# Performance work log

Hardware: AMD Instinct MI355X
Metric: run time of the kernel (lower is better)

Reference implementation:

```python
import jax, jax.numpy as jnp
import numpy as np

B, T, F, H, A, DFF, DEMO, NH = 64, 96, 48, 128, 8, 512, 12, 4
DM = H  # d_model == hidden_dim


def _linear(x, W, b):
    # torch nn.Linear: y = x @ W.T + b, W: [out, in]
    return jnp.einsum('...i,oi->...o', x, W) + b


def _layernorm(x, a, b, eps=1e-7):
    # matches the custom LayerNorm: unbiased std (torch.std default)
    mean = x.mean(-1, keepdims=True)
    std = jnp.std(x, axis=-1, keepdims=True, ddof=1)
    return a * (x - mean) / (std + eps) + b


def _forward(x, demo, gru_Wih, gru_Whh, gru_bih, gru_bhh, att_Wt, att_Wx, att_rate,
             demoW, demob, mWq, mbq, mWk, mbk, mWv, mbv, mWo, mbo,
             ln1_a, ln1_b, ln2_a, ln2_b, ffn_W1, ffn_b1, ffn_W2, ffn_b2,
             fWq, fbq, fWk, fbk, fWv, fbv, outW, outb):
    Bs, Ts, Fs = x.shape
    Hd = gru_Whh.shape[-1]

    # ---- per-feature GRUs (input size 1), vectorized over the F features ----
    def step(h, xt):  # h: [B,F,H], xt: [B,F]
        gi = xt[:, :, None] * gru_Wih[None] + gru_bih[None]            # [B,F,3H]
        gh = jnp.einsum('bfh,fgh->bfg', h, gru_Whh) + gru_bhh[None]    # [B,F,3H]
        ir, iz, inn = jnp.split(gi, 3, -1)
        hr, hz, hn = jnp.split(gh, 3, -1)
        r = jax.nn.sigmoid(ir + hr)
        z = jax.nn.sigmoid(iz + hz)
        n = jnp.tanh(inn + r * hn)
        hnew = (1.0 - z) * n + z * h
        return hnew, hnew

    h0 = jnp.zeros((Bs, Fs, Hd), x.dtype)
    _, Hs = jax.lax.scan(step, h0, jnp.moveaxis(x, 1, 0))  # [T,B,F,H]
    Hs = jnp.moveaxis(Hs, 0, 1)                            # [B,T,F,H]

    # ---- time-aware per-feature attention (SingleAttentionPerFeatureNew) ----
    q = jnp.einsum('bfh,fha->bfa', Hs[:, -1], att_Wt)      # query from last step
    k = jnp.einsum('btfh,fha->btfa', Hs, att_Wx)
    dot = jnp.einsum('bfa,btfa->btf', q, k)                # [B,T,F]
    b_time = jnp.arange(Ts, 0, -1, dtype=x.dtype)[None, :, None]  # T..1
    sr = jax.nn.sigmoid(att_rate)[None, None, :]
    sd = jax.nn.sigmoid(dot)
    denom = sr * (jnp.log(2.72 + (1.0 - sd)) * b_time)
    e = jax.nn.relu(sd / denom)
    a = jax.nn.softmax(e, axis=1)                          # softmax over time
    v = jnp.einsum('btf,btfh->bfh', a, Hs)                 # [B,F,H]

    # ---- demographics channel + concat ----
    demo_main = jnp.tanh(_linear(demo, demoW, demob))[:, None, :]
    posi = jnp.concatenate([v, demo_main], axis=1)         # [B,F+1,H]

    # ---- MHA sublayer (pre-norm residual) with DeCov ----
    xn = _layernorm(posi, ln1_a, ln1_b)
    N = xn.shape[1]
    dk = DM // NH
    qh = _linear(xn, mWq, mbq).reshape(Bs, N, NH, dk).transpose(0, 2, 1, 3)
    kh = _linear(xn, mWk, mbk).reshape(Bs, N, NH, dk).transpose(0, 2, 1, 3)
    vh = _linear(xn, mWv, mbv).reshape(Bs, N, NH, dk).transpose(0, 2, 1, 3)
    scores = jnp.einsum('bhnd,bhmd->bhnm', qh, kh) / jnp.sqrt(jnp.asarray(dk, x.dtype))
    p = jax.nn.softmax(scores, axis=-1)
    ctx = jnp.einsum('bhnm,bhmd->bhnd', p, vh).transpose(0, 2, 1, 3).reshape(Bs, N, DM)
    mha_out = _linear(ctx, mWo, mbo)                       # [B,N,DM]

    # DeCov loss: per position n, covariance across batch, off-diagonal Frobenius
    xc = mha_out - mha_out.mean(axis=0, keepdims=True)     # center over batch
    cov = jnp.einsum('bnh,bng->nhg', xc, xc) / (Bs - 1.0)  # [N,H,H]
    diag = jnp.diagonal(cov, axis1=1, axis2=2)             # [N,H]
    decov = 0.5 * (jnp.sum(cov * cov) - jnp.sum(diag * diag))

    h1 = posi + mha_out

    # ---- FFN sublayer (pre-norm residual) ----
    xn2 = _layernorm(h1, ln2_a, ln2_b)
    ffn = _linear(jax.nn.relu(_linear(xn2, ffn_W1, ffn_b1)), ffn_W2, ffn_b2)
    h2 = h1 + ffn

    # ---- FinalAttentionQKV, attention_type='mul' ----
    fq = _linear(h2[:, -1, :], fWq, fbq)                   # [B,DM]
    fk = _linear(h2, fWk, fbk)                             # [B,N,DM]
    fv = _linear(h2, fWv, fbv)
    fe = jnp.einsum('bna,ba->bn', fk, fq)
    alpha = jax.nn.softmax(fe, axis=1)
    pooled = jnp.einsum('bn,bna->ba', alpha, fv)

    out = jax.nn.sigmoid(_linear(pooled, outW, outb))      # [B,1]
    return out, decov


def setup_inputs() -> dict:
    key = jax.random.key(0)
    ks = jax.random.split(key, 40)
    f32 = jnp.float32

    def rn(k, shape, s=0.05):
        return jax.random.normal(k, shape, dtype=f32) * s

    return {
        'x': jax.random.normal(ks[0], (B, T, F), dtype=f32),
        'demo': jax.random.normal(ks[1], (B, DEMO), dtype=f32),
        'gru_Wih': rn(ks[2], (F, 3 * H)),
        'gru_Whh': rn(ks[3], (F, 3 * H, H)),
        'gru_bih': rn(ks[4], (F, 3 * H)),
        'gru_bhh': rn(ks[5], (F, 3 * H)),
        'att_Wt': rn(ks[6], (F, H, A)),
        'att_Wx': rn(ks[7], (F, H, A)),
        'att_rate': jnp.full((F,), 0.8, dtype=f32),
        'demoW': rn(ks[8], (H, DEMO)), 'demob': rn(ks[9], (H,)),
        'mWq': rn(ks[10], (DM, DM)), 'mbq': rn(ks[11], (DM,)),
        'mWk': rn(ks[12], (DM, DM)), 'mbk': rn(ks[13], (DM,)),
        'mWv': rn(ks[14], (DM, DM)), 'mbv': rn(ks[15], (DM,)),
        'mWo': rn(ks[16], (DM, DM)), 'mbo': rn(ks[17], (DM,)),
        'ln1_a': jnp.ones((DM,), dtype=f32), 'ln1_b': jnp.zeros((DM,), dtype=f32),
        'ln2_a': jnp.ones((DM,), dtype=f32), 'ln2_b': jnp.zeros((DM,), dtype=f32),
        'ffn_W1': rn(ks[18], (DFF, DM)), 'ffn_b1': rn(ks[19], (DFF,)),
        'ffn_W2': rn(ks[20], (DM, DFF)), 'ffn_b2': rn(ks[21], (DM,)),
        'fWq': rn(ks[22], (DM, DM)), 'fbq': rn(ks[23], (DM,)),
        'fWk': rn(ks[24], (DM, DM)), 'fbk': rn(ks[25], (DM,)),
        'fWv': rn(ks[26], (DM, DM)), 'fbv': rn(ks[27], (DM,)),
        'outW': rn(ks[28], (1, DM)), 'outb': rn(ks[29], (1,)),
    }


def reference(x, demo, gru_Wih, gru_Whh, gru_bih, gru_bhh, att_Wt, att_Wx, att_rate,
              demoW, demob, mWq, mbq, mWk, mbk, mWv, mbv, mWo, mbo,
              ln1_a, ln1_b, ln2_a, ln2_b, ffn_W1, ffn_b1, ffn_W2, ffn_b2,
              fWq, fbq, fWk, fbk, fWv, fbv, outW, outb):
    return _forward(x, demo, gru_Wih, gru_Whh, gru_bih, gru_bhh, att_Wt, att_Wx, att_rate,
                    demoW, demob, mWq, mbq, mWk, mbk, mWv, mbv, mWo, mbo,
                    ln1_a, ln1_b, ln2_a, ln2_b, ffn_W1, ffn_b1, ffn_W2, ffn_b2,
                    fWq, fbq, fWk, fbk, fWv, fbv, outW, outb)
```

## Files before the change

### kernel.cpp

```cpp
#include <hip/hip_runtime.h>
#include <hip/hip_bf16.h>

namespace {

constexpr int Bc = 64, Tc = 96, Fc = 48, Hc = 128, Ac = 8;
constexpr int DFFc = 512, DEMOc = 12, NHc = 4, Nc = 49, H3c = 384, DKc = 32;

typedef __attribute__((ext_vector_type(8))) short s8v;
typedef __attribute__((ext_vector_type(4))) float f4v;

__device__ __forceinline__ float sigf(float x) { return 1.f / (1.f + expf(-x)); }
__device__ __forceinline__ float sigf_fast(float x) { return 1.f / (1.f + __expf(-x)); }
__device__ __forceinline__ float tanhf_fast(float x) {
  float e = __expf(2.f * x);
  return 1.f - 2.f / (e + 1.f);
}

__device__ __forceinline__ unsigned short f2b(float v) {
  __hip_bfloat16 h = __float2bfloat16(v);
  union { __hip_bfloat16 b; unsigned short u; } c;
  c.b = h;
  return c.u;
}
__device__ __forceinline__ float b2f(unsigned short u) {
  union { unsigned u32; float f; } c;
  c.u32 = (unsigned)u << 16;
  return c.f;
}

template <typename ST> __device__ __forceinline__ void stv(ST* p, float v);
template <> __device__ __forceinline__ void stv<float>(float* p, float v) { *p = v; }
template <> __device__ __forceinline__ void stv<__hip_bfloat16>(__hip_bfloat16* p, float v) {
  *p = __float2bfloat16(v);
}

template <typename ST> __device__ __forceinline__ void ld4(const ST* p, float* o);
template <> __device__ __forceinline__ void ld4<float>(const float* p, float* o) {
  float4 v = *reinterpret_cast<const float4*>(p);
  o[0] = v.x; o[1] = v.y; o[2] = v.z; o[3] = v.w;
}
template <> __device__ __forceinline__ void ld4<__hip_bfloat16>(const __hip_bfloat16* p, float* o) {
  ushort4 v = *reinterpret_cast<const ushort4*>(p);
  union { unsigned u; float f; } t;
  t.u = (unsigned)v.x << 16; o[0] = t.f;
  t.u = (unsigned)v.y << 16; o[1] = t.f;
  t.u = (unsigned)v.z << 16; o[2] = t.f;
  t.u = (unsigned)v.w << 16; o[3] = t.f;
}

__device__ __forceinline__ float bsum(float v, float* red, int nw) {
#pragma unroll
  for (int off = 32; off > 0; off >>= 1) v += __shfl_down(v, off);
  int lane = threadIdx.x & 63, wid = threadIdx.x >> 6;
  __syncthreads();
  if (lane == 0) red[wid] = v;
  __syncthreads();
  float s = 0.f;
  for (int i = 0; i < nw; i++) s += red[i];
  return s;
}

template <typename ST>
__global__ __launch_bounds__(512, 2) void gru_mfma(
    const float* __restrict__ x, const float* __restrict__ Wih,
    const float* __restrict__ Whh, const float* __restrict__ bih,
    const float* __restrict__ bhh, ST* __restrict__ Hs, float* __restrict__ hT) {
  const int f = blockIdx.x;
  const int b0 = blockIdx.y << 4;
  const int tid = threadIdx.x;
  const int lane = tid & 63;
  const int w = tid >> 6;
  const int hh = (w << 4) + (lane & 15);
  const int lg = lane >> 4;

  s8v wh[12], wl[12];
#pragma unroll
  for (int gate = 0; gate < 3; gate++) {
#pragma unroll
    for (int ks = 0; ks < 4; ks++) {
      const float* wp = Whh + ((size_t)f * H3c + gate * Hc + hh) * Hc + (ks << 5) + (lg << 3);
      s8v hi, lo;
#pragma unroll
      for (int j = 0; j < 8; j++) {
        float v = wp[j];
        unsigned short hb = f2b(v);
        unsigned short lb = f2b(v - b2f(hb));
        hi[j] = (short)hb;
        lo[j] = (short)lb;
      }
      wh[gate * 4 + ks] = hi;
      wl[gate * 4 + ks] = lo;
    }
  }

  const float wi0 = Wih[f * H3c + hh], wi1 = Wih[f * H3c + Hc + hh], wi2 = Wih[f * H3c + 2 * Hc + hh];
  const float bi0 = bih[f * H3c + hh], bi1 = bih[f * H3c + Hc + hh], bi2 = bih[f * H3c + 2 * Hc + hh];
  const float bh0 = bhh[f * H3c + hh], bh1 = bhh[f * H3c + Hc + hh], bh2 = bhh[f * H3c + 2 * Hc + hh];

  __shared__ unsigned short hbuf[2][2][16 * 128];
  __shared__ float xs[16][100];

  {
    unsigned short* hz = &hbuf[0][0][0];
    for (int i = tid; i < 2 * 2 * 16 * 128; i += 512) hz[i] = 0;
    for (int i = tid; i < 16 * Tc; i += 512) {
      int b = i / Tc, t = i - b * Tc;
      xs[b][t] = x[((size_t)(b0 + b) * Tc + t) * Fc + f];
    }
  }
  __syncthreads();

  float hold[4] = {0.f, 0.f, 0.f, 0.f};
  int cur = 0;

  for (int t = 0; t < Tc; t++) {
    s8v ahi[4], alo[4];
#pragma unroll
    for (int ks = 0; ks < 4; ks++) {
      int m = lane & 15;
      int idx = m * 128 + ((((ks << 2) + lg) ^ (m & 7)) << 3);
      ahi[ks] = *reinterpret_cast<const s8v*>(&hbuf[cur][0][idx]);
      alo[ks] = *reinterpret_cast<const s8v*>(&hbuf[cur][1][idx]);
    }
    f4v accr = {0.f, 0.f, 0.f, 0.f}, accz = {0.f, 0.f, 0.f, 0.f}, accn = {0.f, 0.f, 0.f, 0.f};
#pragma unroll
    for (int ks = 0; ks < 4; ks++) {
      accr = __builtin_amdgcn_mfma_f32_16x16x32_bf16(ahi[ks], wh[0 + ks], accr, 0, 0, 0);
      accz = __builtin_amdgcn_mfma_f32_16x16x32_bf16(ahi[ks], wh[4 + ks], accz, 0, 0, 0);
      accn = __builtin_amdgcn_mfma_f32_16x16x32_bf16(ahi[ks], wh[8 + ks], accn, 0, 0, 0);
      accr = __builtin_amdgcn_mfma_f32_16x16x32_bf16(alo[ks], wh[0 + ks], accr, 0, 0, 0);
      accz = __builtin_amdgcn_mfma_f32_16x16x32_bf16(alo[ks], wh[4 + ks], accz, 0, 0, 0);
      accn = __builtin_amdgcn_mfma_f32_16x16x32_bf16(alo[ks], wh[8 + ks], accn, 0, 0, 0);
      accr = __builtin_amdgcn_mfma_f32_16x16x32_bf16(ahi[ks], wl[0 + ks], accr, 0, 0, 0);
      accz = __builtin_amdgcn_mfma_f32_16x16x32_bf16(ahi[ks], wl[4 + ks], accz, 0, 0, 0);
      accn = __builtin_amdgcn_mfma_f32_16x16x32_bf16(ahi[ks], wl[8 + ks], accn, 0, 0, 0);
    }
    int nxt = cur ^ 1;
#pragma unroll
    for (int r = 0; r < 4; r++) {
      int bt = (lg << 2) + r;
      float xv = xs[bt][t];
      float rr = sigf_fast(xv * wi0 + bi0 + accr[r] + bh0);
      float zz = sigf_fast(xv * wi1 + bi1 + accz[r] + bh1);
      float nn = tanhf_fast(xv * wi2 + bi2 + rr * (accn[r] + bh2));
      float hn = (1.f - zz) * nn + zz * hold[r];
      hold[r] = hn;
      stv(&Hs[(((size_t)(b0 + bt) * Tc + t) * Fc + f) * Hc + hh], hn);
      unsigned short hb = f2b(hn);
      unsigned short lb = f2b(hn - b2f(hb));
      int widx = bt * 128 + (((hh >> 3) ^ (bt & 7)) << 3) + (hh & 7);
      hbuf[nxt][0][widx] = hb;
      hbuf[nxt][1][widx] = lb;
    }
    cur = nxt;
    __syncthreads();
  }
#pragma unroll
  for (int r = 0; r < 4; r++) {
    int bt = (lg << 2) + r;
    hT[((size_t)(b0 + bt) * Fc + f) * Hc + hh] = hold[r];
  }
}

template <typename ST>
__global__ __launch_bounds__(256) void feat_attn(
    const ST* __restrict__ Hs, const float* __restrict__ hT,
    const float* __restrict__ Wt, const float* __restrict__ Wx,
    const float* __restrict__ rate, float* __restrict__ posi) {
  const int f = blockIdx.x, b = blockIdx.y;
  const int tid = threadIdx.x;
  __shared__ float tile[Tc][Hc + 1];
  __shared__ float wxs[Hc][Ac];
  __shared__ float qs[Ac];
  __shared__ float es[Tc];
  __shared__ float red[2];

  for (int i = tid; i < Tc * (Hc / 4); i += 256) {
    int t = i >> 5, k = (i & 31) << 2;
    float o[4];
    ld4(&Hs[(((size_t)b * Tc + t) * Fc + f) * Hc + k], o);
    tile[t][k] = o[0]; tile[t][k + 1] = o[1]; tile[t][k + 2] = o[2]; tile[t][k + 3] = o[3];
  }
  for (int i = tid; i < Hc * Ac; i += 256) (&wxs[0][0])[i] = Wx[(size_t)f * Hc * Ac + i];
  if (tid < Ac) {
    float q = 0.f;
    const float* hTp = hT + ((size_t)b * Fc + f) * Hc;
    for (int h = 0; h < Hc; h++) q += hTp[h] * Wt[((size_t)f * Hc + h) * Ac + tid];
    qs[tid] = q;
  }
  __syncthreads();
  if (tid < Tc) {
    float ka[Ac];
#pragma unroll
    for (int a = 0; a < Ac; a++) ka[a] = 0.f;
    for (int h = 0; h < Hc; h++) {
      float hv = tile[tid][h];
#pragma unroll
      for (int a = 0; a < Ac; a++) ka[a] += hv * wxs[h][a];
    }
    float dot = 0.f;
#pragma unroll
    for (int a = 0; a < Ac; a++) dot += qs[a] * ka[a];
    float sd = sigf(dot);
    float denom = sigf(rate[f]) * (logf(2.72f + (1.f - sd)) * (float)(Tc - tid));
    es[tid] = fmaxf(sd / denom, 0.f);
  }
  __syncthreads();
  if (tid == 0) {
    float m = -1e30f;
    for (int t = 0; t < Tc; t++) m = fmaxf(m, es[t]);
    red[0] = m;
  }
  __syncthreads();
  if (tid < Tc) es[tid] = expf(es[tid] - red[0]);
  __syncthreads();
  if (tid == 0) {
    float s = 0.f;
    for (int t = 0; t < Tc; t++) s += es[t];
    red[1] = 1.f / s;
  }
  __syncthreads();
  if (tid < Hc) {
    float acc = 0.f;
    for (int t = 0; t < Tc; t++) acc += es[t] * tile[t][tid];
    posi[((size_t)b * Nc + f) * Hc + tid] = acc * red[1];
  }
}

__global__ __launch_bounds__(128) void demo_k(
    const float* __restrict__ demo, const float* __restrict__ dW,
    const float* __restrict__ db, float* __restrict__ posi) {
  int b = blockIdx.x, h = threadIdx.x;
  float acc = db[h];
  const float* dp = demo + b * DEMOc;
  const float* wp = dW + h * DEMOc;
#pragma unroll
  for (int d = 0; d < DEMOc; d++) acc += dp[d] * wp[d];
  posi[((size_t)b * Nc + (Nc - 1)) * Hc + h] = tanhf(acc);
}

__global__ __launch_bounds__(128) void ln_qkv(
    const float* __restrict__ posi, const float* __restrict__ ga, const float* __restrict__ be,
    const float* __restrict__ Wq, const float* __restrict__ bq,
    const float* __restrict__ Wk, const float* __restrict__ bk,
    const float* __restrict__ Wv, const float* __restrict__ bv,
    float* __restrict__ qb, float* __restrict__ kb, float* __restrict__ vb) {
  int bn = blockIdx.x;
  int b = bn / Nc, n = bn % Nc;
  int h = threadIdx.x;
  __shared__ float xn[Hc];
  __shared__ float red[2];
  float xv = posi[(size_t)bn * Hc + h];
  float m = bsum(xv, red, 2) * (1.f / Hc);
  float d = xv - m;
  float var = bsum(d * d, red, 2) * (1.f / (Hc - 1));
  xn[h] = ga[h] * d / (sqrtf(var) + 1e-7f) + be[h];
  __syncthreads();
  float q = bq[h], k = bk[h], v = bv[h];
  for (int kk = 0; kk < Hc; kk++) {
    float xk = xn[kk];
    q += xk * Wq[h * Hc + kk];
    k += xk * Wk[h * Hc + kk];
    v += xk * Wv[h * Hc + kk];
  }
  int head = h >> 5, dd = h & 31;
  size_t o = (((size_t)b * NHc + head) * Nc + n) * DKc + dd;
  qb[o] = q; kb[o] = k; vb[o] = v;
}

__global__ __launch_bounds__(64) void mha_attn(
    const float* __restrict__ qb, const float* __restrict__ kb,
    const float* __restrict__ vb, float* __restrict__ ctx) {
  int hd = blockIdx.x, b = blockIdx.y;
  int tid = threadIdx.x;
  __shared__ float ksm[Nc][DKc];
  __shared__ float vsm[Nc][DKc];
  __shared__ float sc[Nc][Nc];
  size_t base = ((size_t)b * NHc + hd) * Nc * DKc;
  for (int i = tid; i < Nc * DKc; i += 64) {
    ksm[i / DKc][i % DKc] = kb[base + i];
    vsm[i / DKc][i % DKc] = vb[base + i];
  }
  __syncthreads();
  if (tid < Nc) {
    float qr[DKc];
#pragma unroll
    for (int d = 0; d < DKc; d++) qr[d] = qb[base + tid * DKc + d];
    float mx = -1e30f;
    for (int mm = 0; mm < Nc; mm++) {
      float s = 0.f;
#pragma unroll
      for (int d = 0; d < DKc; d++) s += qr[d] * ksm[mm][d];
      s *= 0.17677669529663687f;
      sc[tid][mm] = s;
      mx = fmaxf(mx, s);
    }
    float ssum = 0.f;
    for (int mm = 0; mm < Nc; mm++) {
      float e = expf(sc[tid][mm] - mx);
      sc[tid][mm] = e;
      ssum += e;
    }
    float inv = 1.f / ssum;
    float acc[DKc];
#pragma unroll
    for (int d = 0; d < DKc; d++) acc[d] = 0.f;
    for (int mm = 0; mm < Nc; mm++) {
      float p = sc[tid][mm] * inv;
#pragma unroll
      for (int d = 0; d < DKc; d++) acc[d] += p * vsm[mm][d];
    }
    float* cp = ctx + ((size_t)b * Nc + tid) * Hc + hd * DKc;
#pragma unroll
    for (int d = 0; d < DKc; d++) cp[d] = acc[d];
  }
}

__global__ __launch_bounds__(128) void wo_res(
    const float* __restrict__ ctx, const float* __restrict__ Wo,
    const float* __restrict__ bo, const float* __restrict__ posi,
    float* __restrict__ mha, float* __restrict__ h1) {
  int bn = blockIdx.x;
  int h = threadIdx.x;
  __shared__ float cs[Hc];
  cs[h] = ctx[(size_t)bn * Hc + h];
  __syncthreads();
  float acc = bo[h];
  for (int k = 0; k < Hc; k++) acc += cs[k] * Wo[h * Hc + k];
  mha[(size_t)bn * Hc + h] = acc;
  h1[(size_t)bn * Hc + h] = posi[(size_t)bn * Hc + h] + acc;
}

__global__ __launch_bounds__(512) void decov_k(
    const float* __restrict__ mha, float* __restrict__ dacc) {
  int n = blockIdx.x;
  int tid = threadIdx.x;
  __shared__ float xc[Bc][Hc];
  __shared__ float red[8];
  for (int i = tid; i < Bc * Hc; i += 512) {
    int b = i >> 7, h = i & 127;
    xc[b][h] = mha[((size_t)b * Nc + n) * Hc + h];
  }
  __syncthreads();
  if (tid < Hc) {
    float s = 0.f;
    for (int b = 0; b < Bc; b++) s += xc[b][tid];
    s *= (1.f / Bc);
    for (int b = 0; b < Bc; b++) xc[b][tid] -= s;
  }
  __syncthreads();
  float p2 = 0.f, pd = 0.f;
  for (int e = tid; e < Hc * Hc; e += 512) {
    int hh = e >> 7, gg = e & 127;
    float c = 0.f;
    for (int b = 0; b < Bc; b++) c += xc[b][hh] * xc[b][gg];
    c *= (1.f / (Bc - 1));
    float c2 = c * c;
    p2 += c2;
    if (hh == gg) pd += c2;
  }
  float s2 = bsum(p2, red, 8);
  float sdg = bsum(pd, red, 8);
  if (tid == 0) atomicAdd(dacc, 0.5f * (s2 - sdg));
}

__global__ __launch_bounds__(256) void ln2_ffn1(
    const float* __restrict__ h1, const float* __restrict__ ga, const float* __restrict__ be,
    const float* __restrict__ W1, const float* __restrict__ b1, float* __restrict__ t1) {
  int bn = blockIdx.x;
  int tid = threadIdx.x;
  __shared__ float xn[Hc];
  __shared__ float red[4];
  float xv = (tid < Hc) ? h1[(size_t)bn * Hc + tid] : 0.f;
  float m = bsum(xv, red, 4) * (1.f / Hc);
  float d = (tid < Hc) ? (xv - m) : 0.f;
  float var = bsum(d * d, red, 4) * (1.f / (Hc - 1));
  if (tid < Hc) xn[tid] = ga[tid] * d / (sqrtf(var) + 1e-7f) + be[tid];
  __syncthreads();
#pragma unroll
  for (int jj = 0; jj < 2; jj++) {
    int j = tid + jj * 256;
    float acc = b1[j];
    for (int k = 0; k < Hc; k++) acc += xn[k] * W1[j * Hc + k];
    t1[(size_t)bn * DFFc + j] = fmaxf(acc, 0.f);
  }
}

__global__ __launch_bounds__(128) void ffn2_res(
    const float* __restrict__ t1, const float* __restrict__ W2,
    const float* __restrict__ b2, const float* __restrict__ h1, float* __restrict__ h2) {
  int bn = blockIdx.x;
  int h = threadIdx.x;
  __shared__ float ts[DFFc];
  for (int i = h; i < DFFc; i += 128) ts[i] = t1[(size_t)bn * DFFc + i];
  __syncthreads();
  float acc = b2[h];
  for (int j = 0; j < DFFc; j++) acc += ts[j] * W2[h * DFFc + j];
  h2[(size_t)bn * Hc + h] = h1[(size_t)bn * Hc + h] + acc;
}

__global__ __launch_bounds__(128) void final_fkv(
    const float* __restrict__ h2,
    const float* __restrict__ Wk, const float* __restrict__ bk,
    const float* __restrict__ Wv, const float* __restrict__ bv,
    const float* __restrict__ Wq, const float* __restrict__ bq,
    float* __restrict__ fkb, float* __restrict__ fvb, float* __restrict__ fqb) {
  int bn = blockIdx.x;
  int b = bn / Nc, n = bn - b * Nc;
  int h = threadIdx.x;
  __shared__ float xs[Hc];
  xs[h] = h2[(size_t)bn * Hc + h];
  __syncthreads();
  float k = bk[h], v = bv[h];
  const float* wkp = Wk + h * Hc;
  const float* wvp = Wv + h * Hc;
  for (int kk = 0; kk < Hc; kk++) {
    float xv = xs[kk];
    k += xv * wkp[kk];
    v += xv * wvp[kk];
  }
  fkb[(size_t)bn * Hc + h] = k;
  fvb[(size_t)bn * Hc + h] = v;
  if (n == Nc - 1) {
    float q = bq[h];
    const float* wqp = Wq + h * Hc;
    for (int kk = 0; kk < Hc; kk++) q += xs[kk] * wqp[kk];
    fqb[(size_t)b * Hc + h] = q;
  }
}

__global__ __launch_bounds__(128) void final2(
    const float* __restrict__ fkb, const float* __restrict__ fvb,
    const float* __restrict__ fqb,
    const float* __restrict__ oW, const float* __restrict__ ob,
    const float* __restrict__ dacc, float* __restrict__ out) {
  int b = blockIdx.x, h = threadIdx.x;
  int lane = h & 63, wid = h >> 6;
  __shared__ float fqs[Hc];
  __shared__ float alphas[Nc];
  __shared__ float red[2];
  __shared__ float r2[2];
  fqs[h] = fqb[(size_t)b * Hc + h];
  __syncthreads();
  for (int n = wid; n < Nc; n += 2) {
    const float* fkp = fkb + ((size_t)b * Nc + n) * Hc;
    float s = fkp[lane] * fqs[lane] + fkp[lane + 64] * fqs[lane + 64];
#pragma unroll
    for (int off = 32; off > 0; off >>= 1) s += __shfl_down(s, off);
    if (lane == 0) alphas[n] = s;
  }
  __syncthreads();
  if (h == 0) {
    float m = -1e30f;
    for (int n = 0; n < Nc; n++) m = fmaxf(m, alphas[n]);
    float ssum = 0.f;
    for (int n = 0; n < Nc; n++) {
      float e = expf(alphas[n] - m);
      alphas[n] = e;
      ssum += e;
    }
    red[0] = 1.f / ssum;
  }
  __syncthreads();
  float inv = red[0];
  float pv = 0.f;
  for (int n = 0; n < Nc; n++) pv += alphas[n] * fvb[((size_t)b * Nc + n) * Hc + h];
  pv *= inv;
  float c = pv * oW[h];
#pragma unroll
  for (int off = 32; off > 0; off >>= 1) c += __shfl_down(c, off);
  if (lane == 0) r2[wid] = c;
  __syncthreads();
  if (h == 0) {
    out[b] = sigf(r2[0] + r2[1] + ob[0]);
    if (b == 0) out[Bc] = dacc[0];
  }
}

}

extern "C" void kernel_launch(void* const* d_in, const int* in_sizes, int n_in,
                              void* d_out, int out_size, void* d_ws, size_t ws_size,
                              hipStream_t stream) {
  const float* x    = (const float*)d_in[0];
  const float* demo = (const float*)d_in[1];
  const float* gWih = (const float*)d_in[2];
  const float* gWhh = (const float*)d_in[3];
  const float* gbih = (const float*)d_in[4];
  const float* gbhh = (const float*)d_in[5];
  const float* aWt  = (const float*)d_in[6];
  const float* aWx  = (const float*)d_in[7];
  const float* aRt  = (const float*)d_in[8];
  const float* dW   = (const float*)d_in[9];
  const float* db   = (const float*)d_in[10];
  const float* mWq  = (const float*)d_in[11];
  const float* mbq  = (const float*)d_in[12];
  const float* mWk  = (const float*)d_in[13];
  const float* mbk  = (const float*)d_in[14];
  const float* mWv  = (const float*)d_in[15];
  const float* mbv  = (const float*)d_in[16];
  const float* mWo  = (const float*)d_in[17];
  const float* mbo  = (const float*)d_in[18];
  const float* l1a  = (const float*)d_in[19];
  const float* l1b  = (const float*)d_in[20];
  const float* l2a  = (const float*)d_in[21];
  const float* l2b  = (const float*)d_in[22];
  const float* fW1  = (const float*)d_in[23];
  const float* fb1  = (const float*)d_in[24];
  const float* fW2  = (const float*)d_in[25];
  const float* fb2  = (const float*)d_in[26];
  const float* fWq  = (const float*)d_in[27];
  const float* fbq  = (const float*)d_in[28];
  const float* fWk  = (const float*)d_in[29];
  const float* fbk  = (const float*)d_in[30];
  const float* fWv  = (const float*)d_in[31];
  const float* fbv  = (const float*)d_in[32];
  const float* oW   = (const float*)d_in[33];
  const float* ob   = (const float*)d_in[34];

  char* base = (char*)d_ws;
  size_t off = 0;
  auto take = [&](size_t nfloats) -> float* {
    float* r = (float*)(base + off);
    off += ((nfloats * sizeof(float)) + 255) & ~(size_t)255;
    return r;
  };
  float* dec  = take(64);
  float* hT   = take((size_t)Bc * Fc * Hc);
  float* posi = take((size_t)Bc * Nc * Hc);
  float* qb   = take((size_t)Bc * Nc * Hc);
  float* kb   = take((size_t)Bc * Nc * Hc);
  float* vb   = take((size_t)Bc * Nc * Hc);
  float* ctx  = take((size_t)Bc * Nc * Hc);
  float* mha  = take((size_t)Bc * Nc * Hc);
  float* h1   = take((size_t)Bc * Nc * Hc);
  float* t1   = take((size_t)Bc * Nc * DFFc);
  float* h2   = take((size_t)Bc * Nc * Hc);
  float* fkb  = take((size_t)Bc * Nc * Hc);
  float* fvb  = take((size_t)Bc * Nc * Hc);
  float* fqb  = take((size_t)Bc * Hc);
  size_t HsElems = (size_t)Bc * Tc * Fc * Hc;
  void* HsPtr = (void*)(base + off);
  bool f32path = (ws_size >= off + HsElems * sizeof(float));

  hipMemsetAsync(dec, 0, sizeof(float), stream);

  dim3 gGru(Fc, Bc / 16);
  dim3 gAtt(Fc, Bc);
  if (f32path) {
    gru_mfma<float><<<gGru, 512, 0, stream>>>(x, gWih, gWhh, gbih, gbhh, (float*)HsPtr, hT);
    feat_attn<float><<<gAtt, 256, 0, stream>>>((const float*)HsPtr, hT, aWt, aWx, aRt, posi);
  } else {
    gru_mfma<__hip_bfloat16><<<gGru, 512, 0, stream>>>(x, gWih, gWhh, gbih, gbhh,
                                                       (__hip_bfloat16*)HsPtr, hT);
    feat_attn<__hip_bfloat16><<<gAtt, 256, 0, stream>>>((const __hip_bfloat16*)HsPtr, hT,
                                                        aWt, aWx, aRt, posi);
  }
  demo_k<<<Bc, 128, 0, stream>>>(demo, dW, db, posi);
  ln_qkv<<<Bc * Nc, 128, 0, stream>>>(posi, l1a, l1b, mWq, mbq, mWk, mbk, mWv, mbv, qb, kb, vb);
  mha_attn<<<dim3(NHc, Bc), 64, 0, stream>>>(qb, kb, vb, ctx);
  wo_res<<<Bc * Nc, 128, 0, stream>>>(ctx, mWo, mbo, posi, mha, h1);
  decov_k<<<Nc, 512, 0, stream>>>(mha, dec);
  ln2_ffn1<<<Bc * Nc, 256, 0, stream>>>(h1, l2a, l2b, fW1, fb1, t1);
  ffn2_res<<<Bc * Nc, 128, 0, stream>>>(t1, fW2, fb2, h1, h2);
  final_fkv<<<Bc * Nc, 128, 0, stream>>>(h2, fWk, fbk, fWv, fbv, fWq, fbq, fkb, fvb, fqb);
  final2<<<Bc, 128, 0, stream>>>(fkb, fvb, fqb, oW, ob, dec, (float*)d_out);
}
```

Measured before the change: 773.2 us.

## Vectorize dense dot products, parallelize attention reductions, split decov, lighter GRU barrier

```diff
diff --git a/kernel.cpp b/kernel.cpp
--- a/kernel.cpp
+++ b/kernel.cpp
@@ -26,6 +26,36 @@
   union { unsigned u32; float f; } c;
   c.u32 = (unsigned)u << 16;
   return c.f;
+}
+
+__device__ __forceinline__ void lds_barrier() {
+  asm volatile("s_waitcnt lgkmcnt(0)" ::: "memory");
+  __builtin_amdgcn_sched_barrier(0);
+  __builtin_amdgcn_s_barrier();
+  __builtin_amdgcn_sched_barrier(0);
+}
+
+__device__ __forceinline__ float dot128(const float* __restrict__ a,
+                                        const float* __restrict__ w) {
+  float s0 = 0.f, s1 = 0.f, s2 = 0.f, s3 = 0.f;
+#pragma unroll
+  for (int k = 0; k < 128; k += 4) {
+    float4 av = *reinterpret_cast<const float4*>(a + k);
+    float4 wv = *reinterpret_cast<const float4*>(w + k);
+    s0 += av.x * wv.x; s1 += av.y * wv.y; s2 += av.z * wv.z; s3 += av.w * wv.w;
+  }
+  return (s0 + s1) + (s2 + s3);
+}
+__device__ __forceinline__ float dot512(const float* __restrict__ a,
+                                        const float* __restrict__ w) {
+  float s0 = 0.f, s1 = 0.f, s2 = 0.f, s3 = 0.f;
+#pragma unroll 8
+  for (int k = 0; k < 512; k += 4) {
+    float4 av = *reinterpret_cast<const float4*>(a + k);
+    float4 wv = *reinterpret_cast<const float4*>(w + k);
+    s0 += av.x * wv.x; s1 += av.y * wv.y; s2 += av.z * wv.z; s3 += av.w * wv.w;
+  }
+  return (s0 + s1) + (s2 + s3);
 }
 
 template <typename ST> __device__ __forceinline__ void stv(ST* p, float v);
@@ -153,7 +183,7 @@
       hbuf[nxt][1][widx] = lb;
     }
     cur = nxt;
-    __syncthreads();
+    lds_barrier();
   }
 #pragma unroll
   for (int r = 0; r < 4; r++) {
@@ -169,11 +199,14 @@
     const float* __restrict__ rate, float* __restrict__ posi) {
   const int f = blockIdx.x, b = blockIdx.y;
   const int tid = threadIdx.x;
+  const int lane = tid & 63, wid = tid >> 6;
   __shared__ float tile[Tc][Hc + 1];
   __shared__ float wxs[Hc][Ac];
   __shared__ float qs[Ac];
   __shared__ float es[Tc];
-  __shared__ float red[2];
+  __shared__ float qpart[2][Ac];
+  __shared__ float red[4];
+  __shared__ float inv_s;
 
   for (int i = tid; i < Tc * (Hc / 4); i += 256) {
     int t = i >> 5, k = (i & 31) << 2;
@@ -182,12 +215,18 @@
     tile[t][k] = o[0]; tile[t][k + 1] = o[1]; tile[t][k + 2] = o[2]; tile[t][k + 3] = o[3];
   }
   for (int i = tid; i < Hc * Ac; i += 256) (&wxs[0][0])[i] = Wx[(size_t)f * Hc * Ac + i];
-  if (tid < Ac) {
-    float q = 0.f;
-    const float* hTp = hT + ((size_t)b * Fc + f) * Hc;
-    for (int h = 0; h < Hc; h++) q += hTp[h] * Wt[((size_t)f * Hc + h) * Ac + tid];
-    qs[tid] = q;
-  }
+  if (tid < Hc) {
+    float hv = hT[((size_t)b * Fc + f) * Hc + tid];
+#pragma unroll
+    for (int a = 0; a < Ac; a++) {
+      float p = hv * Wt[((size_t)f * Hc + tid) * Ac + a];
+#pragma unroll
+      for (int off = 32; off > 0; off >>= 1) p += __shfl_down(p, off);
+      if (lane == 0) qpart[wid][a] = p;
+    }
+  }
+  __syncthreads();
+  if (tid < Ac) qs[tid] = qpart[0][tid] + qpart[1][tid];
   __syncthreads();
   if (tid < Tc) {
     float ka[Ac];
@@ -206,24 +245,31 @@
     es[tid] = fmaxf(sd / denom, 0.f);
   }
   __syncthreads();
-  if (tid == 0) {
-    float m = -1e30f;
-    for (int t = 0; t < Tc; t++) m = fmaxf(m, es[t]);
-    red[0] = m;
-  }
-  __syncthreads();
-  if (tid < Tc) es[tid] = expf(es[tid] - red[0]);
-  __syncthreads();
-  if (tid == 0) {
-    float s = 0.f;
-    for (int t = 0; t < Tc; t++) s += es[t];
-    red[1] = 1.f / s;
-  }
+  float mv = (tid < Tc) ? es[tid] : -1e30f;
+#pragma unroll
+  for (int off = 32; off > 0; off >>= 1) mv = fmaxf(mv, __shfl_down(mv, off));
+  if (lane == 0) red[wid] = mv;
+  __syncthreads();
+  float m = fmaxf(fmaxf(red[0], red[1]), fmaxf(red[2], red[3]));
+  float ev = (tid < Tc) ? __expf(es[tid] - m) : 0.f;
+  if (tid < Tc) es[tid] = ev;
+#pragma unroll
+  for (int off = 32; off > 0; off >>= 1) ev += __shfl_down(ev, off);
+  __syncthreads();
+  if (lane == 0) red[wid] = ev;
+  __syncthreads();
+  if (tid == 0) inv_s = 1.f / (red[0] + red[1] + red[2] + red[3]);
   __syncthreads();
   if (tid < Hc) {
-    float acc = 0.f;
-    for (int t = 0; t < Tc; t++) acc += es[t] * tile[t][tid];
-    posi[((size_t)b * Nc + f) * Hc + tid] = acc * red[1];
+    float s0 = 0.f, s1 = 0.f, s2 = 0.f, s3 = 0.f;
+#pragma unroll
+    for (int t = 0; t < Tc; t += 4) {
+      s0 += es[t] * tile[t][tid];
+      s1 += es[t + 1] * tile[t + 1][tid];
+      s2 += es[t + 2] * tile[t + 2][tid];
+      s3 += es[t + 3] * tile[t + 3][tid];
+    }
+    posi[((size_t)b * Nc + f) * Hc + tid] = ((s0 + s1) + (s2 + s3)) * inv_s;
   }
 }
 
@@ -248,7 +294,7 @@
   int bn = blockIdx.x;
   int b = bn / Nc, n = bn % Nc;
   int h = threadIdx.x;
-  __shared__ float xn[Hc];
+  __shared__ __align__(16) float xn[Hc];
   __shared__ float red[2];
   float xv = posi[(size_t)bn * Hc + h];
   float m = bsum(xv, red, 2) * (1.f / Hc);
@@ -256,13 +302,9 @@
   float var = bsum(d * d, red, 2) * (1.f / (Hc - 1));
   xn[h] = ga[h] * d / (sqrtf(var) + 1e-7f) + be[h];
   __syncthreads();
-  float q = bq[h], k = bk[h], v = bv[h];
-  for (int kk = 0; kk < Hc; kk++) {
-    float xk = xn[kk];
-    q += xk * Wq[h * Hc + kk];
-    k += xk * Wk[h * Hc + kk];
-    v += xk * Wv[h * Hc + kk];
-  }
+  float q = bq[h] + dot128(xn, Wq + h * Hc);
+  float k = bk[h] + dot128(xn, Wk + h * Hc);
+  float v = bv[h] + dot128(xn, Wv + h * Hc);
   int head = h >> 5, dd = h & 31;
   size_t o = (((size_t)b * NHc + head) * Nc + n) * DKc + dd;
   qb[o] = q; kb[o] = k; vb[o] = v;
@@ -322,18 +364,17 @@
     float* __restrict__ mha, float* __restrict__ h1) {
   int bn = blockIdx.x;
   int h = threadIdx.x;
-  __shared__ float cs[Hc];
+  __shared__ __align__(16) float cs[Hc];
   cs[h] = ctx[(size_t)bn * Hc + h];
   __syncthreads();
-  float acc = bo[h];
-  for (int k = 0; k < Hc; k++) acc += cs[k] * Wo[h * Hc + k];
+  float acc = bo[h] + dot128(cs, Wo + h * Hc);
   mha[(size_t)bn * Hc + h] = acc;
   h1[(size_t)bn * Hc + h] = posi[(size_t)bn * Hc + h] + acc;
 }
 
 __global__ __launch_bounds__(512) void decov_k(
     const float* __restrict__ mha, float* __restrict__ dacc) {
-  int n = blockIdx.x;
+  int n = blockIdx.x, q = blockIdx.y;
   int tid = threadIdx.x;
   __shared__ float xc[Bc][Hc];
   __shared__ float red[8];
@@ -350,14 +391,20 @@
   }
   __syncthreads();
   float p2 = 0.f, pd = 0.f;
-  for (int e = tid; e < Hc * Hc; e += 512) {
-    int hh = e >> 7, gg = e & 127;
-    float c = 0.f;
-    for (int b = 0; b < Bc; b++) c += xc[b][hh] * xc[b][gg];
-    c *= (1.f / (Bc - 1));
-    float c2 = c * c;
-    p2 += c2;
-    if (hh == gg) pd += c2;
+  for (int e = tid; e < 32 * Hc; e += 512) {
+    int hh = (q << 5) + (e >> 7), gg = e & 127;
+    float c0 = 0.f, c1 = 0.f, c2 = 0.f, c3 = 0.f;
+#pragma unroll 4
+    for (int b = 0; b < Bc; b += 4) {
+      c0 += xc[b][hh] * xc[b][gg];
+      c1 += xc[b + 1][hh] * xc[b + 1][gg];
+      c2 += xc[b + 2][hh] * xc[b + 2][gg];
+      c3 += xc[b + 3][hh] * xc[b + 3][gg];
+    }
+    float c = ((c0 + c1) + (c2 + c3)) * (1.f / (Bc - 1));
+    float cc = c * c;
+    p2 += cc;
+    if (hh == gg) pd += cc;
   }
   float s2 = bsum(p2, red, 8);
   float sdg = bsum(pd, red, 8);
@@ -369,7 +416,7 @@
     const float* __restrict__ W1, const float* __restrict__ b1, float* __restrict__ t1) {
   int bn = blockIdx.x;
   int tid = threadIdx.x;
-  __shared__ float xn[Hc];
+  __shared__ __align__(16) float xn[Hc];
   __shared__ float red[4];
   float xv = (tid < Hc) ? h1[(size_t)bn * Hc + tid] : 0.f;
   float m = bsum(xv, red, 4) * (1.f / Hc);
@@ -380,8 +427,7 @@
 #pragma unroll
   for (int jj = 0; jj < 2; jj++) {
     int j = tid + jj * 256;
-    float acc = b1[j];
-    for (int k = 0; k < Hc; k++) acc += xn[k] * W1[j * Hc + k];
+    float acc = b1[j] + dot128(xn, W1 + j * Hc);
     t1[(size_t)bn * DFFc + j] = fmaxf(acc, 0.f);
   }
 }
@@ -391,11 +437,10 @@
     const float* __restrict__ b2, const float* __restrict__ h1, float* __restrict__ h2) {
   int bn = blockIdx.x;
   int h = threadIdx.x;
-  __shared__ float ts[DFFc];
+  __shared__ __align__(16) float ts[DFFc];
   for (int i = h; i < DFFc; i += 128) ts[i] = t1[(size_t)bn * DFFc + i];
   __syncthreads();
-  float acc = b2[h];
-  for (int j = 0; j < DFFc; j++) acc += ts[j] * W2[h * DFFc + j];
+  float acc = b2[h] + dot512(ts, W2 + h * DFFc);
   h2[(size_t)bn * Hc + h] = h1[(size_t)bn * Hc + h] + acc;
 }
 
@@ -408,24 +453,13 @@
   int bn = blockIdx.x;
   int b = bn / Nc, n = bn - b * Nc;
   int h = threadIdx.x;
-  __shared__ float xs[Hc];
+  __shared__ __align__(16) float xs[Hc];
   xs[h] = h2[(size_t)bn * Hc + h];
   __syncthreads();
-  float k = bk[h], v = bv[h];
-  const float* wkp = Wk + h * Hc;
-  const float* wvp = Wv + h * Hc;
-  for (int kk = 0; kk < Hc; kk++) {
-    float xv = xs[kk];
-    k += xv * wkp[kk];
-    v += xv * wvp[kk];
-  }
-  fkb[(size_t)bn * Hc + h] = k;
-  fvb[(size_t)bn * Hc + h] = v;
+  fkb[(size_t)bn * Hc + h] = bk[h] + dot128(xs, Wk + h * Hc);
+  fvb[(size_t)bn * Hc + h] = bv[h] + dot128(xs, Wv + h * Hc);
   if (n == Nc - 1) {
-    float q = bq[h];
-    const float* wqp = Wq + h * Hc;
-    for (int kk = 0; kk < Hc; kk++) q += xs[kk] * wqp[kk];
-    fqb[(size_t)b * Hc + h] = q;
+    fqb[(size_t)b * Hc + h] = bq[h] + dot128(xs, Wq + h * Hc);
   }
 }
 
@@ -560,7 +594,7 @@
   ln_qkv<<<Bc * Nc, 128, 0, stream>>>(posi, l1a, l1b, mWq, mbq, mWk, mbk, mWv, mbv, qb, kb, vb);
   mha_attn<<<dim3(NHc, Bc), 64, 0, stream>>>(qb, kb, vb, ctx);
   wo_res<<<Bc * Nc, 128, 0, stream>>>(ctx, mWo, mbo, posi, mha, h1);
-  decov_k<<<Nc, 512, 0, stream>>>(mha, dec);
+  decov_k<<<dim3(Nc, 4), 512, 0, stream>>>(mha, dec);
   ln2_ffn1<<<Bc * Nc, 256, 0, stream>>>(h1, l2a, l2b, fW1, fb1, t1);
   ffn2_res<<<Bc * Nc, 128, 0, stream>>>(t1, fW2, fb2, h1, h2);
   final_fkv<<<Bc * Nc, 128, 0, stream>>>(h2, fWk, fbk, fWv, fbv, fWq, fbq, fkb, fvb, fqb);
```

After: 812.2 us. +5.0%, slower.
